# Optimization experiments

Hardware: AMD Instinct MI355X
Metric: run time of the kernel (lower is better)

The kernel has to match this reference:

```python
import jax, jax.numpy as jnp
import numpy as np

DIM = 1024
NUM_SKILLS = 50


def setup_inputs() -> dict:
    key = jax.random.key(0)
    ks = jax.random.split(key, 7)
    n_tokens = 4096
    scale = 1.0 / np.sqrt(DIM)
    x = jax.random.normal(ks[0], (n_tokens, DIM), dtype=jnp.float32)
    # Stacked expert weights: skill i is Linear(dim,dim) -> ReLU -> Linear(dim,dim)
    W1 = jax.random.uniform(ks[1], (NUM_SKILLS, DIM, DIM), jnp.float32, -scale, scale)
    b1 = jax.random.uniform(ks[2], (NUM_SKILLS, DIM), jnp.float32, -scale, scale)
    W2 = jax.random.uniform(ks[3], (NUM_SKILLS, DIM, DIM), jnp.float32, -scale, scale)
    b2 = jax.random.uniform(ks[4], (NUM_SKILLS, DIM), jnp.float32, -scale, scale)
    # Gating linear: Linear(dim, num_skills)
    Wg = jax.random.uniform(ks[5], (DIM, NUM_SKILLS), jnp.float32, -scale, scale)
    bg = jax.random.uniform(ks[6], (NUM_SKILLS,), jnp.float32, -scale, scale)
    return {"x": x, "W1": W1, "b1": b1, "W2": W2, "b2": b2, "Wg": Wg, "bg": bg}


def reference(x, W1, b1, W2, b2, Wg, bg):
    # Soft-MoE path (skill_id=None): softmax gate over all experts,
    # every expert applied to every token, weighted sum.
    gates = jax.nn.softmax(x @ Wg + bg, axis=-1)            # [n, E]
    h = jax.nn.relu(jnp.einsum('nd,edh->neh', x, W1) + b1)  # [n, E, d]
    y = jnp.einsum('neh,ehd->ned', h, W2) + b2              # [n, E, d]
    out = jnp.einsum('ned,ne->nd', y, gates)                # [n, d]
    return out
```

## Files before the change

### kernel.cpp

```cpp
#include <hip/hip_runtime.h>
#include <stdint.h>

#define AS1 __attribute__((address_space(1)))
#define AS3 __attribute__((address_space(3)))

typedef unsigned short u16;
typedef __attribute__((ext_vector_type(8))) short s16x8;
typedef __attribute__((ext_vector_type(8))) unsigned short u16x8;
typedef __attribute__((ext_vector_type(4))) float f32x4;

__device__ __forceinline__ u16 f2bf(float f) {
    union { float f; unsigned int u; } v; v.f = f;
    unsigned int r = v.u + 0x7fffu + ((v.u >> 16) & 1u);
    return (u16)(r >> 16);
}

__device__ __forceinline__ void gld_lds16(const u16* g, u16* l) {
    __builtin_amdgcn_global_load_lds((AS1 unsigned int*)(uintptr_t)g,
                                     (AS3 unsigned int*)(uintptr_t)l, 16, 0, 0);
}

__global__ void convert_x_kernel(const float* __restrict__ X, u16* __restrict__ Xb, int total8) {
    int i = blockIdx.x * 256 + threadIdx.x;
    if (i < total8) {
        f32x4 a = ((const f32x4*)X)[2 * i];
        f32x4 b = ((const f32x4*)X)[2 * i + 1];
        u16x8 o;
#pragma unroll
        for (int j = 0; j < 4; j++) { o[j] = f2bf(a[j]); o[4 + j] = f2bf(b[j]); }
        ((u16x8*)Xb)[i] = o;
    }
}

__global__ void gate_kernel(const float* __restrict__ X, const float* __restrict__ Wg,
                            const float* __restrict__ bg, float* __restrict__ gates, int nt) {
    __shared__ float xs[1024];
    const int n = blockIdx.x;
    const int t = threadIdx.x;
#pragma unroll
    for (int i = 0; i < 16; i++) xs[t + i * 64] = X[(size_t)n * 1024 + t + i * 64];
    __syncthreads();
    float a = -INFINITY;
    if (t < 50) {
        float s0 = 0.f, s1 = 0.f, s2 = 0.f, s3 = 0.f;
        for (int d = 0; d < 1024; d += 4) {
            s0 += xs[d + 0] * Wg[(d + 0) * 50 + t];
            s1 += xs[d + 1] * Wg[(d + 1) * 50 + t];
            s2 += xs[d + 2] * Wg[(d + 2) * 50 + t];
            s3 += xs[d + 3] * Wg[(d + 3) * 50 + t];
        }
        a = (s0 + s1) + (s2 + s3) + bg[t];
    }
    float m = a;
#pragma unroll
    for (int off = 32; off > 0; off >>= 1) m = fmaxf(m, __shfl_xor(m, off));
    float p = (t < 50) ? __expf(a - m) : 0.f;
    float ss = p;
#pragma unroll
    for (int off = 32; off > 0; off >>= 1) ss += __shfl_xor(ss, off);
    if (t < 50) gates[(size_t)n * 50 + t] = p / ss;
}

__global__ void transpose_kernel(const float* __restrict__ W1s, const float* __restrict__ W2s,
                                 u16* __restrict__ Wt1, u16* __restrict__ Wt2, int eg) {
    __shared__ u16 tile[64 * 65];
    const int t = threadIdx.x;
    const int z = blockIdx.z;
    const float* src; u16* dst;
    if (z < eg) { src = W1s + ((size_t)z << 20); dst = Wt1 + ((size_t)z << 20); }
    else        { src = W2s + ((size_t)(z - eg) << 20); dst = Wt2 + ((size_t)(z - eg) << 20); }
    const int k0 = blockIdx.y * 64;
    const int n0 = blockIdx.x * 64;
#pragma unroll
    for (int p = 0; p < 4; p++) {
        int r = (t >> 4) + 16 * p;
        int c = t & 15;
        f32x4 v = *(const f32x4*)(src + (size_t)(k0 + r) * 1024 + n0 + c * 4);
#pragma unroll
        for (int j = 0; j < 4; j++) tile[r * 65 + c * 4 + j] = f2bf(v[j]);
    }
    __syncthreads();
#pragma unroll
    for (int p = 0; p < 2; p++) {
        int h = (t >> 3) + 32 * p;
        int c = t & 7;
        u16x8 o;
#pragma unroll
        for (int j = 0; j < 8; j++) o[j] = tile[(c * 8 + j) * 65 + h];
        *(u16x8*)(dst + (size_t)(n0 + h) * 1024 + k0 + c * 8) = o;
    }
}


#define BUF_U16 12288

#define STG1(t) { int bo = ((t) % 3) * BUF_U16;                                   \
        const u16* a = Ag + (t) * 32; const u16* b = Bg + (t) * 32;               \
        gld_lds16(a,          Al + bo);                                           \
        gld_lds16(a + 65536,  Al + bo + 2048);                                    \
        gld_lds16(b,          Bl + bo);                                           \
        gld_lds16(b + 65536,  Bl + bo + 2048);                                    \
        gld_lds16(b + 131072, Bl + bo + 4096);                                    \
        gld_lds16(b + 196608, Bl + bo + 6144); }

#define STG2(t) { int kt = kb + (t) * 32; int ee = kt >> 10; int kk = kt & 1023;  \
        const u16* a = Agr + (size_t)ee * ntk + kk;                               \
        const u16* b = Bgr + ((size_t)ee << 20) + kk;                             \
        int bo = ((t) % 3) * BUF_U16;                                             \
        gld_lds16(a,          Al + bo);                                           \
        gld_lds16(a + 65536,  Al + bo + 2048);                                    \
        gld_lds16(b,          Bl + bo);                                           \
        gld_lds16(b + 65536,  Bl + bo + 2048);                                    \
        gld_lds16(b + 131072, Bl + bo + 4096);                                    \
        gld_lds16(b + 196608, Bl + bo + 6144); }

#define MMSTEP(t, VM, DO, STG) {                                                  \
        asm volatile("s_waitcnt vmcnt(" VM ")\n\ts_barrier" ::: "memory");        \
        if (DO) STG((t) + 2);                                                     \
        const u16* bp = smem + ((t) % 3) * BUF_U16;                               \
        s16x8 av[8], bv[4];                                                       \
        _Pragma("unroll") for (int mi = 0; mi < 8; mi++)                          \
            av[mi] = *(const s16x8*)(bp + aoff[mi]);                              \
        _Pragma("unroll") for (int nj = 0; nj < 4; nj++)                          \
            bv[nj] = *(const s16x8*)(bp + boff[nj]);                              \
        __builtin_amdgcn_s_setprio(1);                                            \
        _Pragma("unroll") for (int mi = 0; mi < 8; mi++)                          \
        _Pragma("unroll") for (int nj = 0; nj < 4; nj++)                          \
            acc[mi * 4 + nj] = __builtin_amdgcn_mfma_f32_16x16x32_bf16(           \
                av[mi], bv[nj], acc[mi * 4 + nj], 0, 0, 0);                       \
        __builtin_amdgcn_s_setprio(0); }

__global__ __launch_bounds__(256, 2)
void gemm1_kernel(const u16* __restrict__ X, const u16* __restrict__ Wt1,
                  const float* __restrict__ b1, const float* __restrict__ gates,
                  u16* __restrict__ Hp, int nt, int egbase) {
    __shared__ __align__(16) u16 smem[36864];
    const int tid = threadIdx.x, wave = tid >> 6, lane = tid & 63;
    const int e = blockIdx.z;
    const int m0 = blockIdx.x * 128, n0 = blockIdx.y * 256;

    const int srow = wave * 16 + (lane >> 2);
    const int scg = ((lane & 3) ^ ((srow >> 1) & 3)) * 8;
    const u16* Ag = X + (size_t)(m0 + srow) * 1024 + scg;
    const u16* Bg = Wt1 + ((size_t)e << 20) + (size_t)(n0 + srow) * 1024 + scg;
    u16* Al = smem + wave * 512;
    u16* Bl = smem + 4096 + wave * 512;

    const int fr = lane & 15, fq = lane >> 4;
    int aoff[8], boff[4];
#pragma unroll
    for (int mi = 0; mi < 8; mi++) {
        int ra = mi * 16 + fr;
        aoff[mi] = ra * 32 + ((fq ^ ((ra >> 1) & 3)) * 8);
    }
#pragma unroll
    for (int nj = 0; nj < 4; nj++) {
        int rb = wave * 64 + nj * 16 + fr;
        boff[nj] = 4096 + rb * 32 + ((fq ^ ((rb >> 1) & 3)) * 8);
    }

    f32x4 acc[32];
#pragma unroll
    for (int i = 0; i < 32; i++) acc[i] = (f32x4){0.f, 0.f, 0.f, 0.f};

    STG1(0); STG1(1);
    for (int t = 0; t < 30; ++t) MMSTEP(t, "6", 1, STG1);
    MMSTEP(30, "6", 0, STG1);
    MMSTEP(31, "0", 0, STG1);

    const float* b1e = b1 + (size_t)e * 1024;
    float b1v[4];
#pragma unroll
    for (int nj = 0; nj < 4; nj++) b1v[nj] = b1e[n0 + wave * 64 + nj * 16 + fr];
    const int eglob = egbase + e;

    __syncthreads();
#pragma unroll
    for (int mi = 0; mi < 8; mi++) {
#pragma unroll
        for (int ri = 0; ri < 4; ri++) {
            int row = mi * 16 + fq * 4 + ri;
            float g = gates[(size_t)(m0 + row) * 50 + eglob];
#pragma unroll
            for (int nj = 0; nj < 4; nj++) {
                int col = wave * 64 + nj * 16 + fr;
                float h = acc[mi * 4 + nj][ri] + b1v[nj];
                h = h > 0.f ? h * g : 0.f;
                smem[row * 264 + col] = f2bf(h);
            }
        }
    }
    __syncthreads();
    u16* HpE = Hp + (size_t)e * nt * 1024;
    const int c = tid & 31, rr = tid >> 5;
#pragma unroll
    for (int p = 0; p < 16; p++) {
        int r = rr + p * 8;
        u16x8 v = *(const u16x8*)(smem + r * 264 + c * 8);
        *(u16x8*)(HpE + (size_t)(m0 + r) * 1024 + n0 + c * 8) = v;
    }
}

__global__ __launch_bounds__(256, 2)
void gemm2_kernel(const u16* __restrict__ Hp, const u16* __restrict__ Wt2,
                  float* __restrict__ partial, int nt, int eg, int init) {
    __shared__ __align__(16) u16 smem[36864];
    const int tid = threadIdx.x, wave = tid >> 6, lane = tid & 63;
    const int s = blockIdx.z;
    const int m0 = blockIdx.x * 128, n0 = blockIdx.y * 256;

    const int srow = wave * 16 + (lane >> 2);
    const int scg = ((lane & 3) ^ ((srow >> 1) & 3)) * 8;
    const u16* Agr = Hp + (size_t)(m0 + srow) * 1024 + scg;
    const u16* Bgr = Wt2 + (size_t)(n0 + srow) * 1024 + scg;
    const size_t ntk = (size_t)nt * 1024;
    u16* Al = smem + wave * 512;
    u16* Bl = smem + 4096 + wave * 512;

    const int fr = lane & 15, fq = lane >> 4;
    int aoff[8], boff[4];
#pragma unroll
    for (int mi = 0; mi < 8; mi++) {
        int ra = mi * 16 + fr;
        aoff[mi] = ra * 32 + ((fq ^ ((ra >> 1) & 3)) * 8);
    }
#pragma unroll
    for (int nj = 0; nj < 4; nj++) {
        int rb = wave * 64 + nj * 16 + fr;
        boff[nj] = 4096 + rb * 32 + ((fq ^ ((rb >> 1) & 3)) * 8);
    }

    f32x4 acc[32];
#pragma unroll
    for (int i = 0; i < 32; i++) acc[i] = (f32x4){0.f, 0.f, 0.f, 0.f};

    const int NT = eg * 8;
    const int kb = s * NT * 32;

    STG2(0); STG2(1);
    for (int t = 0; t < NT - 2; ++t) MMSTEP(t, "6", 1, STG2);
    MMSTEP(NT - 2, "6", 0, STG2);
    MMSTEP(NT - 1, "0", 0, STG2);

    float* pp = partial + (size_t)s * nt * 1024;
#pragma unroll
    for (int mi = 0; mi < 8; mi++) {
#pragma unroll
        for (int ri = 0; ri < 4; ri++) {
            int gr = m0 + mi * 16 + fq * 4 + ri;
#pragma unroll
            for (int nj = 0; nj < 4; nj++) {
                size_t idx = (size_t)gr * 1024 + n0 + wave * 64 + nj * 16 + fr;
                float v = acc[mi * 4 + nj][ri];
                if (!init) v += pp[idx];
                pp[idx] = v;
            }
        }
    }
}

__global__ void finalize_kernel(const float* __restrict__ partial, const float* __restrict__ gates,
                                const float* __restrict__ b2, float* __restrict__ out, int nt) {
    __shared__ float gs[50];
    const int n = blockIdx.x;
    const int t = threadIdx.x;
    if (t < 50) gs[t] = gates[(size_t)n * 50 + t];
    __syncthreads();
    const size_t base = (size_t)n * 1024;
    const size_t st = (size_t)nt * 1024;
#pragma unroll
    for (int i = 0; i < 4; i++) {
        int d = t + i * 256;
        float v = partial[base + d] + partial[st + base + d]
                + partial[2 * st + base + d] + partial[3 * st + base + d];
#pragma unroll 10
        for (int e2 = 0; e2 < 50; e2++) v += gs[e2] * b2[e2 * 1024 + d];
        out[base + d] = v;
    }
}

extern "C" void kernel_launch(void* const* d_in, const int* in_sizes, int n_in,
                              void* d_out, int out_size, void* d_ws, size_t ws_size,
                              hipStream_t stream) {
    const float* x  = (const float*)d_in[0];
    const float* W1 = (const float*)d_in[1];
    const float* b1 = (const float*)d_in[2];
    const float* W2 = (const float*)d_in[3];
    const float* b2 = (const float*)d_in[4];
    const float* Wg = (const float*)d_in[5];
    const float* bg = (const float*)d_in[6];
    float* out = (float*)d_out;
    const int nt = in_sizes[0] / 1024;

    char* w = (char*)d_ws;
    auto carve = [&](size_t bytes) -> char* {
        char* p = w; w += (bytes + 255) & ~(size_t)255; return p;
    };
    float* gates   = (float*)carve((size_t)nt * 50 * 4);
    float* partial = (float*)carve((size_t)4 * nt * 1024 * 4);
    u16*   xb      = (u16*)carve((size_t)nt * 1024 * 2);
    const size_t fixed = (size_t)(w - (char*)d_ws);

    int eg = 1;
    const int cand[6] = {50, 25, 10, 5, 2, 1};
    for (int i = 0; i < 6; i++) {
        size_t need = fixed + (size_t)cand[i] * ((size_t)2 * 2097152 + (size_t)nt * 1024 * 2) + 4096;
        if (need <= ws_size) { eg = cand[i]; break; }
    }
    u16* Wt1 = (u16*)carve((size_t)eg * 1048576 * 2);
    u16* Wt2 = (u16*)carve((size_t)eg * 1048576 * 2);
    u16* Hp  = (u16*)carve((size_t)eg * nt * 1024 * 2);

    convert_x_kernel<<<(nt * 1024 / 8 + 255) / 256, 256, 0, stream>>>(x, xb, nt * 1024 / 8);
    gate_kernel<<<nt, 64, 0, stream>>>(x, Wg, bg, gates, nt);

    const int groups = 50 / eg;
    for (int g = 0; g < groups; ++g) {
        transpose_kernel<<<dim3(16, 16, 2 * eg), 256, 0, stream>>>(
            W1 + ((size_t)(g * eg) << 20), W2 + ((size_t)(g * eg) << 20), Wt1, Wt2, eg);
        gemm1_kernel<<<dim3(nt / 128, 4, eg), 256, 0, stream>>>(
            xb, Wt1, b1 + (size_t)g * eg * 1024, gates, Hp, nt, g * eg);
        gemm2_kernel<<<dim3(nt / 128, 4, 4), 256, 0, stream>>>(
            Hp, Wt2, partial, nt, eg, g == 0 ? 1 : 0);
    }
    finalize_kernel<<<nt, 256, 0, stream>>>(partial, gates, b2, out, nt);
}
```

Measured before the change: 1.427 ms.

## Double-buffer LDS fragments in registers to overlap LDS reads with MFMA

Restructures the GEMM main loops in both kernels so that the LDS fragments for the next K tile are loaded into a second register set while the MFMAs run on the current set, alternating fa/fb. Each step now waits for all outstanding global-to-LDS loads (vmcnt(0)) before issuing the next stage, and the per-fragment LDS offset arrays are replaced by a single base plus constant strides. This is meant to hide LDS read latency behind matrix math. In exchange it roughly doubles the fragment register footprint and shortens how far global loads can run ahead, which could add spills or more memory stalls.

```diff
diff --git a/kernel.cpp b/kernel.cpp
--- a/kernel.cpp
+++ b/kernel.cpp
@@ -94,40 +94,42 @@
 
 #define BUF_U16 12288
 
-#define STG1(t) { int bo = ((t) % 3) * BUF_U16;                                   \
+#define STG1(t, bo) {                                                             \
         const u16* a = Ag + (t) * 32; const u16* b = Bg + (t) * 32;               \
-        gld_lds16(a,          Al + bo);                                           \
-        gld_lds16(a + 65536,  Al + bo + 2048);                                    \
-        gld_lds16(b,          Bl + bo);                                           \
-        gld_lds16(b + 65536,  Bl + bo + 2048);                                    \
-        gld_lds16(b + 131072, Bl + bo + 4096);                                    \
-        gld_lds16(b + 196608, Bl + bo + 6144); }
-
-#define STG2(t) { int kt = kb + (t) * 32; int ee = kt >> 10; int kk = kt & 1023;  \
+        gld_lds16(a,          Al + (bo));                                         \
+        gld_lds16(a + 65536,  Al + (bo) + 2048);                                  \
+        gld_lds16(b,          Bl + (bo));                                         \
+        gld_lds16(b + 65536,  Bl + (bo) + 2048);                                  \
+        gld_lds16(b + 131072, Bl + (bo) + 4096);                                  \
+        gld_lds16(b + 196608, Bl + (bo) + 6144); }
+
+#define STG2(t, bo) { int kt = kb + (t) * 32; int ee = kt >> 10; int kk = kt & 1023; \
         const u16* a = Agr + (size_t)ee * ntk + kk;                               \
         const u16* b = Bgr + ((size_t)ee << 20) + kk;                             \
-        int bo = ((t) % 3) * BUF_U16;                                             \
-        gld_lds16(a,          Al + bo);                                           \
-        gld_lds16(a + 65536,  Al + bo + 2048);                                    \
-        gld_lds16(b,          Bl + bo);                                           \
-        gld_lds16(b + 65536,  Bl + bo + 2048);                                    \
-        gld_lds16(b + 131072, Bl + bo + 4096);                                    \
-        gld_lds16(b + 196608, Bl + bo + 6144); }
-
-#define MMSTEP(t, VM, DO, STG) {                                                  \
-        asm volatile("s_waitcnt vmcnt(" VM ")\n\ts_barrier" ::: "memory");        \
-        if (DO) STG((t) + 2);                                                     \
-        const u16* bp = smem + ((t) % 3) * BUF_U16;                               \
-        s16x8 av[8], bv[4];                                                       \
-        _Pragma("unroll") for (int mi = 0; mi < 8; mi++)                          \
-            av[mi] = *(const s16x8*)(bp + aoff[mi]);                              \
-        _Pragma("unroll") for (int nj = 0; nj < 4; nj++)                          \
-            bv[nj] = *(const s16x8*)(bp + boff[nj]);                              \
+        gld_lds16(a,          Al + (bo));                                         \
+        gld_lds16(a + 65536,  Al + (bo) + 2048);                                  \
+        gld_lds16(b,          Bl + (bo));                                         \
+        gld_lds16(b + 65536,  Bl + (bo) + 2048);                                  \
+        gld_lds16(b + 131072, Bl + (bo) + 4096);                                  \
+        gld_lds16(b + 196608, Bl + (bo) + 6144); }
+
+#define MMSTEP(t, DORD, DOSTG, STG, FC, FN) {                                     \
+        asm volatile("s_waitcnt vmcnt(0)\n\ts_barrier" ::: "memory");             \
+        if (DORD) {                                                               \
+            const u16* bp = smem + bn * BUF_U16;                                  \
+            _Pragma("unroll") for (int mi = 0; mi < 8; mi++)                      \
+                FN[mi] = *(const s16x8*)(bp + abase + mi * 512);                  \
+            _Pragma("unroll") for (int nj = 0; nj < 4; nj++)                      \
+                FN[8 + nj] = *(const s16x8*)(bp + bbase + nj * 512);              \
+        }                                                                         \
+        { int bs = (bn == 2) ? 0 : bn + 1;                                        \
+          if (DOSTG) STG((t) + 2, bs * BUF_U16);                                  \
+          bn = bs; }                                                              \
         __builtin_amdgcn_s_setprio(1);                                            \
         _Pragma("unroll") for (int mi = 0; mi < 8; mi++)                          \
         _Pragma("unroll") for (int nj = 0; nj < 4; nj++)                          \
             acc[mi * 4 + nj] = __builtin_amdgcn_mfma_f32_16x16x32_bf16(           \
-                av[mi], bv[nj], acc[mi * 4 + nj], 0, 0, 0);                       \
+                FC[mi], FC[8 + nj], acc[mi * 4 + nj], 0, 0, 0);                   \
         __builtin_amdgcn_s_setprio(0); }
 
 __global__ __launch_bounds__(256, 2)
@@ -147,26 +149,31 @@
     u16* Bl = smem + 4096 + wave * 512;
 
     const int fr = lane & 15, fq = lane >> 4;
-    int aoff[8], boff[4];
-#pragma unroll
-    for (int mi = 0; mi < 8; mi++) {
-        int ra = mi * 16 + fr;
-        aoff[mi] = ra * 32 + ((fq ^ ((ra >> 1) & 3)) * 8);
-    }
-#pragma unroll
-    for (int nj = 0; nj < 4; nj++) {
-        int rb = wave * 64 + nj * 16 + fr;
-        boff[nj] = 4096 + rb * 32 + ((fq ^ ((rb >> 1) & 3)) * 8);
-    }
+    const int swz = (fq ^ ((fr >> 1) & 3)) * 8;
+    const int abase = fr * 32 + swz;
+    const int bbase = 4096 + (wave * 64 + fr) * 32 + swz;
 
     f32x4 acc[32];
 #pragma unroll
     for (int i = 0; i < 32; i++) acc[i] = (f32x4){0.f, 0.f, 0.f, 0.f};
 
-    STG1(0); STG1(1);
-    for (int t = 0; t < 30; ++t) MMSTEP(t, "6", 1, STG1);
-    MMSTEP(30, "6", 0, STG1);
-    MMSTEP(31, "0", 0, STG1);
+    s16x8 fa[12], fb[12];
+
+    STG1(0, 0); STG1(1, BUF_U16);
+    asm volatile("s_waitcnt vmcnt(6)\n\ts_barrier" ::: "memory");
+    {
+        const u16* bp = smem;
+#pragma unroll
+        for (int mi = 0; mi < 8; mi++) fa[mi] = *(const s16x8*)(bp + abase + mi * 512);
+#pragma unroll
+        for (int nj = 0; nj < 4; nj++) fa[8 + nj] = *(const s16x8*)(bp + bbase + nj * 512);
+    }
+    int bn = 1;
+#pragma unroll 2
+    for (int t = 0; t < 32; t += 2) {
+        MMSTEP(t,     1,          t + 2 < 32, STG1, fa, fb);
+        MMSTEP(t + 1, t + 2 < 32, t + 3 < 32, STG1, fb, fa);
+    }
 
     const float* b1e = b1 + (size_t)e * 1024;
     float b1v[4];
@@ -218,17 +225,9 @@
     u16* Bl = smem + 4096 + wave * 512;
 
     const int fr = lane & 15, fq = lane >> 4;
-    int aoff[8], boff[4];
-#pragma unroll
-    for (int mi = 0; mi < 8; mi++) {
-        int ra = mi * 16 + fr;
-        aoff[mi] = ra * 32 + ((fq ^ ((ra >> 1) & 3)) * 8);
-    }
-#pragma unroll
-    for (int nj = 0; nj < 4; nj++) {
-        int rb = wave * 64 + nj * 16 + fr;
-        boff[nj] = 4096 + rb * 32 + ((fq ^ ((rb >> 1) & 3)) * 8);
-    }
+    const int swz = (fq ^ ((fr >> 1) & 3)) * 8;
+    const int abase = fr * 32 + swz;
+    const int bbase = 4096 + (wave * 64 + fr) * 32 + swz;
 
     f32x4 acc[32];
 #pragma unroll
@@ -237,10 +236,22 @@
     const int NT = eg * 8;
     const int kb = s * NT * 32;
 
-    STG2(0); STG2(1);
-    for (int t = 0; t < NT - 2; ++t) MMSTEP(t, "6", 1, STG2);
-    MMSTEP(NT - 2, "6", 0, STG2);
-    MMSTEP(NT - 1, "0", 0, STG2);
+    s16x8 fa[12], fb[12];
+
+    STG2(0, 0); STG2(1, BUF_U16);
+    asm volatile("s_waitcnt vmcnt(6)\n\ts_barrier" ::: "memory");
+    {
+        const u16* bp = smem;
+#pragma unroll
+        for (int mi = 0; mi < 8; mi++) fa[mi] = *(const s16x8*)(bp + abase + mi * 512);
+#pragma unroll
+        for (int nj = 0; nj < 4; nj++) fa[8 + nj] = *(const s16x8*)(bp + bbase + nj * 512);
+    }
+    int bn = 1;
+    for (int t = 0; t < NT; t += 2) {
+        MMSTEP(t,     1,          t + 2 < NT, STG2, fa, fb);
+        MMSTEP(t + 1, t + 2 < NT, t + 3 < NT, STG2, fb, fa);
+    }
 
     float* pp = partial + (size_t)s * nt * 1024;
 #pragma unroll
```

Result: slower. 2.031 ms (+42.3%).
